# Kernel optimization log

Hardware: AMD Instinct MI355X
Metric: run time of the kernel (lower is better)

Reference implementation:

```python
import jax, jax.numpy as jnp
import numpy as np

B, T, C = 4, 2048, 2048
H = 16
DH = C // H  # 128
ROPE_BASE = 10000.0


def _rms_norm(x):
    eps = jnp.finfo(x.dtype).eps
    return x * jax.lax.rsqrt(jnp.mean(x * x, axis=-1, keepdims=True) + eps)


def _rope_tables(seq_len, dim, dtype):
    inv_freq = 1.0 / (ROPE_BASE ** (jnp.arange(0, dim, 2, dtype=jnp.float32) / dim))
    t = jnp.arange(seq_len, dtype=jnp.float32)
    freqs = jnp.outer(t, inv_freq)  # [T, dim/2]
    return jnp.cos(freqs).astype(dtype), jnp.sin(freqs).astype(dtype)


def _apply_rotary(x, cos, sin):
    # x: [B, T, H, DH]; cos/sin: [T, DH/2] broadcast over batch and heads
    d = x.shape[-1] // 2
    x1, x2 = x[..., :d], x[..., d:]
    c = cos[None, :, None, :]
    s = sin[None, :, None, :]
    y1 = x1 * c + x2 * s
    y2 = -x1 * s + x2 * c
    return jnp.concatenate([y1, y2], axis=-1).astype(x.dtype)


def setup_inputs() -> dict:
    key = jax.random.key(0)
    k0, k1, k2, k3, k4 = jax.random.split(key, 5)
    scale = 1.0 / np.sqrt(C)
    return {
        "residual": jax.random.normal(k0, (B, T, C), dtype=jnp.float32),
        "wq": jax.random.normal(k1, (C, C), dtype=jnp.float32) * scale,
        "wk": jax.random.normal(k2, (C, C), dtype=jnp.float32) * scale,
        "wv": jax.random.normal(k3, (C, C), dtype=jnp.float32) * scale,
        "wproj": jax.random.normal(k4, (C, C), dtype=jnp.float32) * scale,
    }


def reference(residual, wq, wk, wv, wproj):
    x = _rms_norm(residual)  # [B, T, C]
    # torch Linear: y = x @ W.T, W is [out, in]
    q = jnp.einsum('btc,dc->btd', x, wq).reshape(B, T, H, DH)
    k = jnp.einsum('btc,dc->btd', x, wk).reshape(B, T, H, DH)
    v = jnp.einsum('btc,dc->btd', x, wv).reshape(B, T, H, DH)
    # per-head QK RMSNorm
    q = _rms_norm(q)
    k = _rms_norm(k)
    cos, sin = _rope_tables(T, DH, residual.dtype)
    q = _apply_rotary(q, cos, sin)
    k = _apply_rotary(k, cos, sin)
    # causal attention, scale 1/sqrt(head_dim)
    scores = jnp.einsum('bqhd,bkhd->bhqk', q, k) / jnp.sqrt(jnp.asarray(DH, q.dtype))
    causal = jnp.tril(jnp.ones((T, T), dtype=bool))
    scores = jnp.where(causal[None, None], scores, jnp.asarray(-jnp.inf, scores.dtype))
    attn = jax.nn.softmax(scores, axis=-1)
    y = jnp.einsum('bhqk,bkhd->bqhd', attn, v).reshape(B, T, C)
    y = jnp.einsum('btc,dc->btd', y, wproj)
    return residual + y
```

## Files before the change

kernel.cpp:

```cpp
#include <hip/hip_runtime.h>
#include <hip/hip_bf16.h>

#define B_  4
#define T_  2048
#define C_  2048
#define H_  16
#define DH_ 128
#define MROWS (B_ * T_)

typedef unsigned short bf16;
typedef __attribute__((ext_vector_type(8))) short bf16x8;
typedef __attribute__((ext_vector_type(4))) float f32x4;

__device__ __forceinline__ float bf2f(bf16 h) {
    return __uint_as_float(((unsigned int)h) << 16);
}
__device__ __forceinline__ bf16 f2bf(float f) {
    unsigned int u = __float_as_uint(f);
    u = (u + 0x7fffu + ((u >> 16) & 1u)) >> 16;
    return (bf16)u;
}

__device__ __forceinline__ int swz8(int row, int col) {
    return col ^ ((row & 7) << 3);
}

__device__ __forceinline__ void gld16(const bf16* g, bf16* l) {
    __builtin_amdgcn_global_load_lds(
        (const __attribute__((address_space(1))) unsigned int*)(const unsigned int*)g,
        (__attribute__((address_space(3))) unsigned int*)(unsigned int*)l,
        16, 0, 0);
}

__global__ __launch_bounds__(256) void w2bf(const float* __restrict__ w, bf16* __restrict__ o) {
    const size_t i = ((size_t)blockIdx.x * 256 + threadIdx.x) * 8;
    float4 a = *(const float4*)(w + i);
    float4 b = *(const float4*)(w + i + 4);
    union { uint4 u; bf16 h[8]; } p;
    p.h[0] = f2bf(a.x); p.h[1] = f2bf(a.y); p.h[2] = f2bf(a.z); p.h[3] = f2bf(a.w);
    p.h[4] = f2bf(b.x); p.h[5] = f2bf(b.y); p.h[6] = f2bf(b.z); p.h[7] = f2bf(b.w);
    *(uint4*)(o + i) = p.u;
}

__global__ __launch_bounds__(256) void rmsnorm_x(const float* __restrict__ in,
                                                 bf16* __restrict__ outx) {
    const int row = blockIdx.x, tid = threadIdx.x;
    const size_t base = (size_t)row * C_ + tid * 8;
    float4 a = *(const float4*)(in + base);
    float4 b = *(const float4*)(in + base + 4);
    float f[8] = {a.x, a.y, a.z, a.w, b.x, b.y, b.z, b.w};
    float ss = 0.f;
#pragma unroll
    for (int i = 0; i < 8; ++i) ss += f[i] * f[i];
#pragma unroll
    for (int m = 32; m; m >>= 1) ss += __shfl_xor(ss, m, 64);
    __shared__ float red[4];
    if ((tid & 63) == 0) red[tid >> 6] = ss;
    __syncthreads();
    float tot = red[0] + red[1] + red[2] + red[3];
    float sc = rsqrtf(tot * (1.0f / (float)C_) + 1.1920929e-07f);
    union { uint4 u; bf16 h[8]; } o;
#pragma unroll
    for (int i = 0; i < 8; ++i) o.h[i] = f2bf(f[i] * sc);
    *(uint4*)(outx + base) = o.u;
}

template <int MODE>
__global__ __launch_bounds__(256, 2)
void gemm_bt(const bf16* __restrict__ A, const bf16* __restrict__ W,
             void* __restrict__ Dv, const float* __restrict__ Add) {
    __shared__ __align__(16) bf16 sA[128 * 64];
    __shared__ __align__(16) bf16 sB[128 * 64];
    const int tid = threadIdx.x;
    const int w = tid >> 6, L = tid & 63;
    const int lane15 = L & 15, quad = L >> 4;
    const int m0 = blockIdx.x * 128, n0 = blockIdx.y * 128;
    const int wm = w >> 1, wn = w & 1;

    const bf16* aptr[4];
    const bf16* bptr[4];
#pragma unroll
    for (int it = 0; it < 4; ++it) {
        int slot = it * 256 + tid;
        int row = slot >> 3;
        int ch = slot & 7;
        aptr[it] = A + (size_t)(m0 + row) * C_ + ch * 8;
        bptr[it] = W + (size_t)(n0 + row) * C_ + ch * 8;
    }

    f32x4 acc[4][4] = {};
#pragma unroll 1
    for (int kt = 0; kt < C_ / 64; ++kt) {
        __syncthreads();
#pragma unroll
        for (int it = 0; it < 4; ++it) {
            gld16(aptr[it], sA + (size_t)(it * 256 + w * 64) * 8);
            aptr[it] += 64;
        }
#pragma unroll
        for (int it = 0; it < 4; ++it) {
            gld16(bptr[it], sB + (size_t)(it * 256 + w * 64) * 8);
            bptr[it] += 64;
        }
        __syncthreads();
#pragma unroll
        for (int ks = 0; ks < 2; ++ks) {
            bf16x8 af[4], bfr[4];
#pragma unroll
            for (int i = 0; i < 4; ++i) {
                int ar = wm * 64 + i * 16 + lane15;
                af[i]  = *(const bf16x8*)(sA + ar * 64 + (ks * 4 + quad) * 8);
                int br = wn * 64 + i * 16 + lane15;
                bfr[i] = *(const bf16x8*)(sB + br * 64 + (ks * 4 + quad) * 8);
            }
#pragma unroll
            for (int i = 0; i < 4; ++i)
#pragma unroll
                for (int j = 0; j < 4; ++j)
                    acc[i][j] = __builtin_amdgcn_mfma_f32_16x16x32_bf16(af[i], bfr[j], acc[i][j], 0, 0, 0);
        }
    }

    if (MODE == 2) {
        bf16* D = (bf16*)Dv;
#pragma unroll
        for (int i = 0; i < 4; ++i) {
            int t0 = m0 + wm * 64 + i * 16 + quad * 4;
            int bidx = t0 >> 11, tin = t0 & (T_ - 1);
#pragma unroll
            for (int j = 0; j < 4; ++j) {
                int col = n0 + wn * 64 + j * 16 + lane15;
                int hh = col >> 7, dh = col & (DH_ - 1);
                unsigned int lo = (unsigned int)f2bf(acc[i][j][0]) | ((unsigned int)f2bf(acc[i][j][1]) << 16);
                unsigned int hi = (unsigned int)f2bf(acc[i][j][2]) | ((unsigned int)f2bf(acc[i][j][3]) << 16);
                uint2 val; val.x = lo; val.y = hi;
                *(uint2*)(D + ((size_t)((bidx * H_ + hh) * DH_ + dh)) * T_ + tin) = val;
            }
        }
    } else if (MODE == 1) {
        float* D = (float*)Dv;
#pragma unroll
        for (int i = 0; i < 4; ++i)
#pragma unroll
            for (int j = 0; j < 4; ++j)
#pragma unroll
                for (int r = 0; r < 4; ++r) {
                    int row = m0 + wm * 64 + i * 16 + quad * 4 + r;
                    int col = n0 + wn * 64 + j * 16 + lane15;
                    D[(size_t)row * C_ + col] = acc[i][j][r] + Add[(size_t)row * C_ + col];
                }
    } else {
        bf16* D = (bf16*)Dv;
#pragma unroll
        for (int i = 0; i < 4; ++i)
#pragma unroll
            for (int j = 0; j < 4; ++j)
#pragma unroll
                for (int r = 0; r < 4; ++r) {
                    int row = m0 + wm * 64 + i * 16 + quad * 4 + r;
                    int col = n0 + wn * 64 + j * 16 + lane15;
                    D[(size_t)row * C_ + col] = f2bf(acc[i][j][r]);
                }
    }
}

__global__ __launch_bounds__(256) void qknorm_rope(bf16* __restrict__ q, bf16* __restrict__ k) {
    const int bt = blockIdx.x;
    bf16* buf = blockIdx.y ? k : q;
    const int w = threadIdx.x >> 6, L = threadIdx.x & 63;
    const int t = bt & (T_ - 1);
    float inv = (float)exp2(-(double)L * 0.20762050593046006);
    float ang = (float)t * inv;
    float s, c;
    sincosf(ang, &s, &c);
#pragma unroll
    for (int hh = 0; hh < 4; ++hh) {
        int h = w * 4 + hh;
        bf16* p = buf + (size_t)bt * C_ + h * DH_;
        float x1 = bf2f(p[L]), x2 = bf2f(p[L + 64]);
        float ss = x1 * x1 + x2 * x2;
#pragma unroll
        for (int m = 32; m; m >>= 1) ss += __shfl_xor(ss, m, 64);
        float sc = rsqrtf(ss * (1.0f / (float)DH_) + 1.1920929e-07f);
        float y1 = (x1 * c + x2 * s) * sc;
        float y2 = (x2 * c - x1 * s) * sc;
        p[L]      = f2bf(y1);
        p[L + 64] = f2bf(y2);
    }
}

__global__ __launch_bounds__(256, 3)
void attn_fwd(const bf16* __restrict__ q, const bf16* __restrict__ k,
              const bf16* __restrict__ vt, bf16* __restrict__ y) {
    __shared__ __align__(16) bf16 sK[64 * 128];
    __shared__ __align__(16) bf16 sV[128 * 64];
    __shared__ __align__(16) bf16 sP[128 * 64];
    const int qt = (int)gridDim.x - 1 - (int)blockIdx.x;
    const int bh = blockIdx.y;
    const int b = bh >> 4, h = bh & 15;
    const int tid = threadIdx.x;
    const int w = tid >> 6, L = tid & 63;
    const int lane15 = L & 15, quad = L >> 4;
    const float SCALE = 0.08838834764831845f;

    const bf16* kbase = k  + ((size_t)(b * T_)) * C_ + h * DH_;
    const bf16* vbase = vt + ((size_t)bh * DH_) * T_;

    bf16x8 qf[2][4];
#pragma unroll
    for (int nt = 0; nt < 2; ++nt)
#pragma unroll
        for (int ks = 0; ks < 4; ++ks) {
            int qrow = qt * 128 + w * 32 + nt * 16 + lane15;
            qf[nt][ks] = *(const bf16x8*)(q + ((size_t)(b * T_ + qrow)) * C_ + h * DH_ + ks * 32 + quad * 8);
        }

    f32x4 o[2][8] = {};
    float m_i[2] = {-__builtin_inff(), -__builtin_inff()};
    float l_i[2] = {0.f, 0.f};

    const int jlast = 2 * qt + 1;

#define STAGE_KV(jj)                                                                  \
    do {                                                                              \
        const int base_ = (jj) * 64;                                                  \
        _Pragma("unroll")                                                             \
        for (int it = 0; it < 4; ++it) {                                              \
            int slot = it * 256 + tid;                                                \
            int row = slot >> 4, ch = slot & 15;                                      \
            gld16(kbase + (size_t)(base_ + row) * C_ + ((ch ^ (row & 7)) << 3),       \
                  sK + (size_t)(it * 256 + w * 64) * 8);                              \
        }                                                                             \
        _Pragma("unroll")                                                             \
        for (int it = 0; it < 4; ++it) {                                              \
            int slot = it * 256 + tid;                                                \
            int row = slot >> 3, ch = slot & 7;                                       \
            gld16(vbase + (size_t)row * T_ + base_ + ((ch ^ (row & 7)) << 3),         \
                  sV + (size_t)(it * 256 + w * 64) * 8);                              \
        }                                                                             \
    } while (0)

    for (int jj = 0; jj <= jlast; ++jj) {
        __syncthreads();
        STAGE_KV(jj);
        __syncthreads();

        const bool skip = (jj == jlast) && (w < 2);
        if (!skip) {
            f32x4 sc[4][2] = {};
            __builtin_amdgcn_s_setprio(1);
#pragma unroll
            for (int ks = 0; ks < 4; ++ks)
#pragma unroll
                for (int mt = 0; mt < 4; ++mt) {
                    int ar = mt * 16 + lane15;
                    bf16x8 a = *(const bf16x8*)(sK + ar * 128 + (((ks * 4 + quad) ^ (ar & 7)) << 3));
                    sc[mt][0] = __builtin_amdgcn_mfma_f32_16x16x32_bf16(a, qf[0][ks], sc[mt][0], 0, 0, 0);
                    sc[mt][1] = __builtin_amdgcn_mfma_f32_16x16x32_bf16(a, qf[1][ks], sc[mt][1], 0, 0, 0);
                }
            __builtin_amdgcn_s_setprio(0);

            const bool diag = (jj == 2 * qt && w < 2) || (jj == jlast && w >= 2);
            float alpha[2];
            bool needv[2];
#pragma unroll
            for (int nt = 0; nt < 2; ++nt) {
                const int qr = qt * 128 + w * 32 + nt * 16 + lane15;
                float mx = -__builtin_inff();
#pragma unroll
                for (int mt = 0; mt < 4; ++mt)
#pragma unroll
                    for (int r = 0; r < 4; ++r) {
                        float v = sc[mt][nt][r] * SCALE;
                        if (diag) {
                            int kr = jj * 64 + mt * 16 + quad * 4 + r;
                            if (kr > qr) v = -__builtin_inff();
                        }
                        sc[mt][nt][r] = v;
                        mx = fmaxf(mx, v);
                    }
                mx = fmaxf(mx, __shfl_xor(mx, 16));
                mx = fmaxf(mx, __shfl_xor(mx, 32));
                bool nd = __any(mx > m_i[nt] + 8.0f) != 0;
                float mn = nd ? fmaxf(m_i[nt], mx) : m_i[nt];
                alpha[nt] = nd ? __expf(m_i[nt] - mn) : 1.0f;
                needv[nt] = nd;
                float sum = 0.f;
#pragma unroll
                for (int mt = 0; mt < 4; ++mt)
#pragma unroll
                    for (int r = 0; r < 4; ++r) {
                        float p = __expf(sc[mt][nt][r] - mn);
                        sc[mt][nt][r] = p;
                        sum += p;
                    }
                sum += __shfl_xor(sum, 16);
                sum += __shfl_xor(sum, 32);
                l_i[nt] = l_i[nt] * alpha[nt] + sum;
                m_i[nt] = mn;
            }

#pragma unroll
            for (int mt = 0; mt < 4; ++mt)
#pragma unroll
                for (int nt = 0; nt < 2; ++nt) {
                    int prow = w * 32 + nt * 16 + lane15;
                    int kr0 = mt * 16 + quad * 4;
                    int off = prow * 64 + ((((kr0 >> 3) ^ (prow & 7)) << 3) | (kr0 & 7));
                    unsigned int lo = (unsigned int)f2bf(sc[mt][nt][0]) | ((unsigned int)f2bf(sc[mt][nt][1]) << 16);
                    unsigned int hi = (unsigned int)f2bf(sc[mt][nt][2]) | ((unsigned int)f2bf(sc[mt][nt][3]) << 16);
                    uint2 val; val.x = lo; val.y = hi;
                    *(uint2*)(sP + off) = val;
                }

#pragma unroll
            for (int g = 0; g < 2; ++g)
                if (needv[g]) {
#pragma unroll
                    for (int r = 0; r < 4; ++r) {
                        float av = __shfl(alpha[g], quad * 4 + r, 64);
#pragma unroll
                        for (int d = 0; d < 8; ++d) o[g][d][r] *= av;
                    }
                }

            __builtin_amdgcn_s_setprio(1);
#pragma unroll
            for (int ks = 0; ks < 2; ++ks) {
                bf16x8 ap[2];
#pragma unroll
                for (int g = 0; g < 2; ++g) {
                    int pr = w * 32 + g * 16 + lane15;
                    ap[g] = *(const bf16x8*)(sP + pr * 64 + (((ks * 4 + quad) ^ (pr & 7)) << 3));
                }
#pragma unroll
                for (int d = 0; d < 8; ++d) {
                    int vr = d * 16 + lane15;
                    bf16x8 bv = *(const bf16x8*)(sV + vr * 64 + (((ks * 4 + quad) ^ (vr & 7)) << 3));
                    o[0][d] = __builtin_amdgcn_mfma_f32_16x16x32_bf16(ap[0], bv, o[0][d], 0, 0, 0);
                    o[1][d] = __builtin_amdgcn_mfma_f32_16x16x32_bf16(ap[1], bv, o[1][d], 0, 0, 0);
                }
            }
            __builtin_amdgcn_s_setprio(0);
        }
    }
#undef STAGE_KV

    float rl[2] = {1.f / l_i[0], 1.f / l_i[1]};
#pragma unroll
    for (int g = 0; g < 2; ++g)
#pragma unroll
        for (int r = 0; r < 4; ++r) {
            float linv = __shfl(rl[g], quad * 4 + r, 64);
            int t = qt * 128 + w * 32 + g * 16 + quad * 4 + r;
#pragma unroll
            for (int d = 0; d < 8; ++d)
                y[((size_t)(b * T_ + t)) * C_ + h * DH_ + d * 16 + lane15] = f2bf(o[g][d][r] * linv);
        }
}

extern "C" void kernel_launch(void* const* d_in, const int* in_sizes, int n_in,
                              void* d_out, int out_size, void* d_ws, size_t ws_size,
                              hipStream_t stream) {
    const float* residual = (const float*)d_in[0];
    const float* wq    = (const float*)d_in[1];
    const float* wk    = (const float*)d_in[2];
    const float* wv    = (const float*)d_in[3];
    const float* wproj = (const float*)d_in[4];

    const size_t NE = (size_t)B_ * T_ * C_;
    const size_t WE = (size_t)C_ * C_;
    bf16* x  = (bf16*)d_ws;
    bf16* q  = x + NE;
    bf16* vt = q + NE;
    bf16* kk = (bf16*)d_out;
    bf16* wqb = kk + NE;
    bf16* wkb = wqb + WE;
    bf16* wvb = wkb + WE;
    bf16* y  = x;
    bf16* wpb = q;

    const dim3 gemm_grid(MROWS / 128, C_ / 128);
    const int wgrid = (int)(WE / (256 * 8));

    w2bf<<<wgrid, 256, 0, stream>>>(wq, wqb);
    w2bf<<<wgrid, 256, 0, stream>>>(wk, wkb);
    w2bf<<<wgrid, 256, 0, stream>>>(wv, wvb);
    rmsnorm_x<<<MROWS, 256, 0, stream>>>(residual, x);
    gemm_bt<0><<<gemm_grid, 256, 0, stream>>>(x, wqb, q,  nullptr);
    gemm_bt<0><<<gemm_grid, 256, 0, stream>>>(x, wkb, kk, nullptr);
    gemm_bt<2><<<gemm_grid, 256, 0, stream>>>(x, wvb, vt, nullptr);
    qknorm_rope<<<dim3(MROWS, 2), 256, 0, stream>>>(q, kk);
    attn_fwd<<<dim3(T_ / 128, B_ * H_), 256, 0, stream>>>(q, kk, vt, y);
    w2bf<<<wgrid, 256, 0, stream>>>(wproj, wpb);
    gemm_bt<1><<<gemm_grid, 256, 0, stream>>>(y, wpb, d_out, residual);
}
```

Measured before the change: 845.9 us.

## Register-prefetch next KV tile during compute and remap blocks for L2 locality

```diff
diff --git a/kernel.cpp b/kernel.cpp
--- a/kernel.cpp
+++ b/kernel.cpp
@@ -19,10 +19,6 @@
     unsigned int u = __float_as_uint(f);
     u = (u + 0x7fffu + ((u >> 16) & 1u)) >> 16;
     return (bf16)u;
-}
-
-__device__ __forceinline__ int swz8(int row, int col) {
-    return col ^ ((row & 7) << 3);
 }
 
 __device__ __forceinline__ void gld16(const bf16* g, bf16* l) {
@@ -195,16 +191,23 @@
     __shared__ __align__(16) bf16 sK[64 * 128];
     __shared__ __align__(16) bf16 sV[128 * 64];
     __shared__ __align__(16) bf16 sP[128 * 64];
-    const int qt = (int)gridDim.x - 1 - (int)blockIdx.x;
-    const int bh = blockIdx.y;
-    const int b = bh >> 4, h = bh & 15;
     const int tid = threadIdx.x;
     const int w = tid >> 6, L = tid & 63;
     const int lane15 = L & 15, quad = L >> 4;
     const float SCALE = 0.08838834764831845f;
 
+    const int fid = (int)blockIdx.y * (int)gridDim.x + (int)blockIdx.x;
+    const int bh = (fid & 7) + ((fid >> 7) << 3);
+    const int qt = 15 - ((fid >> 3) & 15);
+    const int b = bh >> 4, h = bh & 15;
+
     const bf16* kbase = k  + ((size_t)(b * T_)) * C_ + h * DH_;
     const bf16* vbase = vt + ((size_t)bh * DH_) * T_;
+
+    const int kch = tid & 15, krow0 = tid >> 4;
+    const int vch = tid & 7,  vrow0 = tid >> 3;
+    const int kldsoff = krow0 * 128 + ((kch ^ (krow0 & 7)) << 3);
+    const int vldsoff = vrow0 * 64  + ((vch ^ (vrow0 & 7)) << 3);
 
     bf16x8 qf[2][4];
 #pragma unroll
@@ -221,29 +224,28 @@
 
     const int jlast = 2 * qt + 1;
 
-#define STAGE_KV(jj)                                                                  \
-    do {                                                                              \
-        const int base_ = (jj) * 64;                                                  \
-        _Pragma("unroll")                                                             \
-        for (int it = 0; it < 4; ++it) {                                              \
-            int slot = it * 256 + tid;                                                \
-            int row = slot >> 4, ch = slot & 15;                                      \
-            gld16(kbase + (size_t)(base_ + row) * C_ + ((ch ^ (row & 7)) << 3),       \
-                  sK + (size_t)(it * 256 + w * 64) * 8);                              \
-        }                                                                             \
-        _Pragma("unroll")                                                             \
-        for (int it = 0; it < 4; ++it) {                                              \
-            int slot = it * 256 + tid;                                                \
-            int row = slot >> 3, ch = slot & 7;                                       \
-            gld16(vbase + (size_t)row * T_ + base_ + ((ch ^ (row & 7)) << 3),         \
-                  sV + (size_t)(it * 256 + w * 64) * 8);                              \
-        }                                                                             \
+    uint4 kreg[4], vreg[4];
+#define LOAD_KV(jj)                                                                      \
+    do {                                                                                 \
+        const int base_ = (jj) * 64;                                                     \
+        _Pragma("unroll")                                                                \
+        for (int it = 0; it < 4; ++it) {                                                 \
+            kreg[it] = *(const uint4*)(kbase + (size_t)(base_ + krow0 + it * 16) * C_ + kch * 8); \
+            vreg[it] = *(const uint4*)(vbase + (size_t)(vrow0 + it * 32) * T_ + base_ + vch * 8); \
+        }                                                                                \
     } while (0)
+
+    LOAD_KV(0);
 
     for (int jj = 0; jj <= jlast; ++jj) {
         __syncthreads();
-        STAGE_KV(jj);
+#pragma unroll
+        for (int it = 0; it < 4; ++it) {
+            *(uint4*)(sK + kldsoff + it * (16 * 128)) = kreg[it];
+            *(uint4*)(sV + vldsoff + it * (32 * 64))  = vreg[it];
+        }
         __syncthreads();
+        if (jj < jlast) LOAD_KV(jj + 1);
 
         const bool skip = (jj == jlast) && (w < 2);
         if (!skip) {
@@ -344,7 +346,7 @@
             __builtin_amdgcn_s_setprio(0);
         }
     }
-#undef STAGE_KV
+#undef LOAD_KV
 
     float rl[2] = {1.f / l_i[0], 1.f / l_i[1]};
 #pragma unroll
```

Result: no change. 855.9 us (+1.2%).
